# Optimization experiments

Hardware: AMD Instinct MI355X
Metric: run time of the kernel (lower is better)

## Reference

```python
import jax, jax.numpy as jnp
import numpy as np

M_IND = 1024   # inducing points
K_NN = 16      # nearest neighbors
JITTER = 1e-4


def rbf(X, Z):
    # unit-variance, unit-lengthscale RBF kernel; returns (K, squared distances)
    sq = jnp.sum(X * X, -1)[:, None] + jnp.sum(Z * Z, -1)[None, :] - 2.0 * (X @ Z.T)
    sq = jnp.maximum(sq, 0.0)
    return jnp.exp(-0.5 * sq), sq


def setup_inputs() -> dict:
    key = jax.random.key(0)
    k1, k2, k3 = jax.random.split(key, 3)
    return {
        "X": jax.random.normal(k1, (65536, 3), jnp.float32),
        "Z": jax.random.normal(k2, (M_IND, 3), jnp.float32),
        "Lu_raw": jax.random.normal(k3, (M_IND, M_IND), jnp.float32),
        "mu": jnp.zeros((M_IND,), jnp.float32),
    }


def reference(X, Z, Lu_raw, mu):
    N = X.shape[0]
    Kxx = jnp.ones((N,), X.dtype)                      # diag of RBF(X,X) is 1
    Kxz, dist = rbf(X, Z)                              # [N,M], [N,M]
    Kzz, _ = rbf(Z, Z)                                 # [M,M]

    # transform_to(lower_cholesky): strict lower triangle + exp(diag)
    Lu = jnp.tril(Lu_raw, -1) + jnp.diag(jnp.exp(jnp.diag(Lu_raw)))

    eyeM = jnp.eye(M_IND, dtype=X.dtype)
    L = jnp.linalg.cholesky(Kzz + JITTER * eyeM)       # [M,M]
    Kzz_j = L @ L.T                                    # == little_L @ little_L.T math (Kzz + jitter*I)
    Su = Lu @ Lu.T                                     # full variational covariance

    # K nearest inducing points per data point (argsort(dist)[:, :K])
    _, idx = jax.lax.top_k(-dist, K_NN)                # [N,K]

    lKzz = Kzz_j[idx[:, :, None], idx[:, None, :]]     # [N,K,K] gathered submatrices
    lS = Su[idx[:, :, None], idx[:, None, :]]          # [N,K,K]
    lKxz = jnp.take_along_axis(Kxz, idx, axis=1)       # [N,K]
    lmu = mu[idx]                                      # [N,K]

    eyeK = jnp.eye(K_NN, dtype=X.dtype)
    inv = jnp.linalg.inv(lKzz + JITTER * eyeK)         # batched tiny inverses [N,K,K]
    W = jnp.einsum('nk,nkj->nj', lKxz, inv)            # [N,K]

    mean = jnp.einsum('nk,nk->n', W, lmu)              # [N]
    cov = (Kxx
           - jnp.einsum('ni,nij,nj->n', W, lKzz, W)
           + jnp.einsum('ni,nij,nj->n', W, lS, W))
    std = jnp.sqrt(jnp.clip(cov, 0.05, None))          # qF scale = clamp(cov, 0.05)**0.5
    return jnp.stack([mean, std])                      # [2,N] qF parameters
```

## Files before the change

kernel.cpp:

```cpp
#include <hip/hip_runtime.h>
#include <math.h>

#define N_PTS 65536
#define M_IND 1024
#define KNN 16
#define JITTER 1e-4f

#define PACKED_FLOATS (M_IND * (M_IND + 1) / 2)
#define PACKED_BYTES  ((size_t)PACKED_FLOATS * sizeof(float))

#define TSU 32
#define SU_BLOCKS 528
#define PTS_PER_BLK 128
#define QSTRIDE 17
#define GRID_BLKS (N_PTS / PTS_PER_BLK)

__device__ __forceinline__ void su_tile(const float* __restrict__ Lu_raw,
                                        float* __restrict__ P,
                                        int bid, int tid,
                                        float (*As)[36], float (*Bs)[36]) {
    int rt = (int)((sqrtf(8.0f * (float)bid + 1.0f) - 1.0f) * 0.5f);
    while ((rt + 1) * (rt + 2) / 2 <= bid) ++rt;
    while (rt * (rt + 1) / 2 > bid) --rt;
    int ct = bid - rt * (rt + 1) / 2;
    int i0 = rt * TSU, j0 = ct * TSU;

    int tx = tid & 15, ty = tid >> 4;
    int sr = tid >> 3, sc = (tid & 7) << 2;
    float a00 = 0.f, a01 = 0.f, a10 = 0.f, a11 = 0.f;

    int nch = ct + 1;
    int gi = i0 + sr, gj = j0 + sr;
    float4 pa = *(const float4*)(Lu_raw + (unsigned)gi * M_IND + sc);
    float4 pb = *(const float4*)(Lu_raw + (unsigned)gj * M_IND + sc);

    for (int c = 0; c < nch; ++c) {
        int gk = (c << 5) + sc;
        float aa[4] = {pa.x, pa.y, pa.z, pa.w};
        float bb[4] = {pb.x, pb.y, pb.z, pb.w};
        #pragma unroll
        for (int q = 0; q < 4; ++q) {
            int k = gk + q;
            aa[q] = (k < gi) ? aa[q] : ((k == gi) ? __expf(aa[q]) : 0.0f);
            bb[q] = (k < gj) ? bb[q] : ((k == gj) ? __expf(bb[q]) : 0.0f);
        }
        *(float4*)&As[sr][sc] = make_float4(aa[0], aa[1], aa[2], aa[3]);
        *(float4*)&Bs[sr][sc] = make_float4(bb[0], bb[1], bb[2], bb[3]);
        __syncthreads();
        if (c + 1 < nch) {
            int kn = ((c + 1) << 5) + sc;
            pa = *(const float4*)(Lu_raw + (unsigned)gi * M_IND + kn);
            pb = *(const float4*)(Lu_raw + (unsigned)gj * M_IND + kn);
        }
        #pragma unroll
        for (int kk = 0; kk < 32; kk += 4) {
            float4 av0 = *(const float4*)&As[ty][kk];
            float4 av1 = *(const float4*)&As[ty + 16][kk];
            float4 bv0 = *(const float4*)&Bs[tx][kk];
            float4 bv1 = *(const float4*)&Bs[tx + 16][kk];
            a00 = fmaf(av0.x, bv0.x, fmaf(av0.y, bv0.y, fmaf(av0.z, bv0.z, fmaf(av0.w, bv0.w, a00))));
            a01 = fmaf(av0.x, bv1.x, fmaf(av0.y, bv1.y, fmaf(av0.z, bv1.z, fmaf(av0.w, bv1.w, a01))));
            a10 = fmaf(av1.x, bv0.x, fmaf(av1.y, bv0.y, fmaf(av1.z, bv0.z, fmaf(av1.w, bv0.w, a10))));
            a11 = fmaf(av1.x, bv1.x, fmaf(av1.y, bv1.y, fmaf(av1.z, bv1.z, fmaf(av1.w, bv1.w, a11))));
        }
        __syncthreads();
    }

    int ia = i0 + ty, ib = i0 + ty + 16;
    int ja = j0 + tx, jb = j0 + tx + 16;
    if (ja <= ia) P[((unsigned)ia * (ia + 1) >> 1) + ja] = a00;
    if (jb <= ia) P[((unsigned)ia * (ia + 1) >> 1) + jb] = a01;
    if (ja <= ib) P[((unsigned)ib * (ib + 1) >> 1) + ja] = a10;
    if (jb <= ib) P[((unsigned)ib * (ib + 1) >> 1) + jb] = a11;
}

__global__ __launch_bounds__(256) void su_kernel(const float* __restrict__ Lu_raw,
                                                 float* __restrict__ P) {
    __shared__ float As[TSU][36];
    __shared__ float Bs[TSU][36];
    su_tile(Lu_raw, P, blockIdx.x, threadIdx.x, As, Bs);
}

__device__ __forceinline__ void ce(unsigned long long& x, unsigned long long& y) {
    unsigned long long a = x, b = y;
    bool c = a < b;
    x = c ? a : b;
    y = c ? b : a;
}
__device__ __forceinline__ void ce(float& x, float& y) {
    float a = fminf(x, y), b = fmaxf(x, y);
    x = a; y = b;
}

template <typename KT>
__device__ __forceinline__ void sort16(KT* a) {
    #pragma unroll
    for (int p = 1; p < 16; p <<= 1)
        #pragma unroll
        for (int k = p; k >= 1; k >>= 1)
            #pragma unroll
            for (int j = k & (p - 1); j + k < 16; j += 2 * k)
                #pragma unroll
                for (int i = 0; i < k; ++i)
                    if (i + j + k < 16)
                        if (((i + j) / (2 * p)) == ((i + j + k) / (2 * p)))
                            ce(a[i + j], a[i + j + k]);
}

template <typename KT>
__device__ __forceinline__ void cleanup16(KT* a) {
    #pragma unroll
    for (int d = 8; d >= 1; d >>= 1)
        #pragma unroll
        for (int i = 0; i < 16; ++i)
            if ((i & d) == 0) ce(a[i], a[i | d]);
}

__device__ __forceinline__ float distf(float4 z, float x0, float x1, float x2, float xq) {
    float dot = fmaf(x0, z.x, fmaf(x1, z.y, x2 * z.z));
    return fmaxf(fmaf(-2.0f, dot, xq + z.w), 0.0f);
}

template <int MODE>
__global__ __launch_bounds__(256, 2) void vnngp_kernel(const float* __restrict__ X,
                                                       const float* __restrict__ Z,
                                                       const float* __restrict__ mu,
                                                       float* __restrict__ P,
                                                       const float* __restrict__ Lu_raw,
                                                       unsigned int* __restrict__ ctr,
                                                       float* __restrict__ out) {
    __shared__ __align__(16) char smem[37888];
    float4* Zs = (float4*)smem;
    float* mus = (float*)(smem + 16384);
    unsigned long long* qb = (unsigned long long*)(smem + 20480);
    int tid = threadIdx.x;

    for (int r = tid; r < M_IND; r += 256) {
        float zx = Z[r * 3 + 0], zy = Z[r * 3 + 1], zz = Z[r * 3 + 2];
        Zs[r] = make_float4(zx, zy, zz, zx * zx + zy * zy + zz * zz);
        mus[r] = mu[r];
    }

    if (MODE == 2) {
        float (*As)[36] = (float (*)[36])(smem + 20480);
        float (*Bs)[36] = (float (*)[36])(smem + 20480 + 4608);
        int t = blockIdx.x;
        #pragma unroll
        for (int r = 16; r < 32; ++r) {
            int s = (r * (r + 1)) >> 1;
            if (t >= s) ++t;
        }
        su_tile(Lu_raw, P, t, tid, As, Bs);
        if (blockIdx.x < 16) {
            int r = 16 + blockIdx.x;
            su_tile(Lu_raw, P, (r * (r + 1)) >> 1, tid, As, Bs);
        }
        __syncthreads();
        if (tid == 0) {
            __threadfence();
            atomicAdd(ctr, 1u);
        }
    } else {
        __syncthreads();
    }

    {
        int pt = tid >> 2, sub = tid & 3;
        int nA = blockIdx.x * PTS_PER_BLK + pt;
        int nB = nA + 64;
        float xA0 = X[nA * 3 + 0], xA1 = X[nA * 3 + 1], xA2 = X[nA * 3 + 2];
        float xB0 = X[nB * 3 + 0], xB1 = X[nB * 3 + 1], xB2 = X[nB * 3 + 2];
        float xqA = fmaf(xA0, xA0, fmaf(xA1, xA1, xA2 * xA2));
        float xqB = fmaf(xB0, xB0, fmaf(xB1, xB1, xB2 * xB2));
        int mbase = sub << 8;
        int rot = sub << 1;

        float TA[16], TB[16];
        #pragma unroll
        for (int j = 0; j < 16; ++j) { TA[j] = 3.4e38f; TB[j] = 3.4e38f; }
        #pragma unroll 1
        for (int c = 0; c < 16; ++c) {
            int base = mbase + (c << 4);
            #pragma unroll
            for (int j = 0; j < 16; ++j) {
                int m = base + ((j + rot) & 15);
                float4 z = Zs[m];
                TA[j] = fminf(TA[j], distf(z, xA0, xA1, xA2, xqA));
                TB[j] = fminf(TB[j], distf(z, xB0, xB1, xB2, xqB));
            }
        }
        sort16(TA);
        sort16(TB);
        #pragma unroll
        for (int round = 1; round <= 2; round <<= 1) {
            float oA[16], oB[16];
            #pragma unroll
            for (int i = 0; i < 16; ++i) {
                oA[i] = __shfl_xor(TA[i], round, 64);
                oB[i] = __shfl_xor(TB[i], round, 64);
            }
            #pragma unroll
            for (int i = 0; i < 16; ++i) {
                TA[i] = fminf(TA[i], oA[15 - i]);
                TB[i] = fminf(TB[i], oB[15 - i]);
            }
            cleanup16(TA);
            cleanup16(TB);
        }
        float TstarA = TA[15], TstarB = TB[15];

        unsigned short* mycA = ((unsigned short*)qb) + pt * (QSTRIDE * 4) + sub * 16;
        unsigned short* mycB = ((unsigned short*)qb) + (pt + 64) * (QSTRIDE * 4) + sub * 16;
        int cntA = 0, cntB = 0;
        #pragma unroll 1
        for (int c = 0; c < 16; ++c) {
            int base = mbase + (c << 4);
            #pragma unroll
            for (int j = 0; j < 16; ++j) {
                int m = base + ((j + rot) & 15);
                float4 z = Zs[m];
                float dA = distf(z, xA0, xA1, xA2, xqA);
                float dB = distf(z, xB0, xB1, xB2, xqB);
                if (dA <= TstarA) { if (cntA < 16) mycA[cntA] = (unsigned short)m; ++cntA; }
                if (dB <= TstarB) { if (cntB < 16) mycB[cntB] = (unsigned short)m; ++cntB; }
            }
        }

        int ovfA = cntA > 16 ? 1 : 0;
        ovfA |= __shfl_xor(ovfA, 1, 64);
        ovfA |= __shfl_xor(ovfA, 2, 64);
        int ovfB = cntB > 16 ? 1 : 0;
        ovfB |= __shfl_xor(ovfB, 1, 64);
        ovfB |= __shfl_xor(ovfB, 2, 64);

        if (!ovfA) {
            const unsigned long long* m64 = (const unsigned long long*)mycA;
            unsigned long long raw[4] = {m64[0], m64[1], m64[2], m64[3]};
            unsigned long long C[16];
            #pragma unroll
            for (int i = 0; i < 16; ++i) {
                int m = (int)((raw[i >> 2] >> ((i & 3) * 16)) & 0x3FF);
                float d = distf(Zs[m], xA0, xA1, xA2, xqA);
                unsigned long long key =
                    ((unsigned long long)__float_as_uint(d) << 32) | (unsigned)m;
                C[i] = (i < cntA) ? key : ~0ULL;
            }
            sort16(C);
            #pragma unroll
            for (int round = 1; round <= 2; round <<= 1) {
                unsigned long long o[16];
                #pragma unroll
                for (int i = 0; i < 16; ++i) o[i] = __shfl_xor(C[i], round, 64);
                #pragma unroll
                for (int i = 0; i < 16; ++i) {
                    unsigned long long b = o[15 - i];
                    C[i] = C[i] < b ? C[i] : b;
                }
                cleanup16(C);
            }
            if (sub == 0) {
                #pragma unroll
                for (int i = 0; i < 16; ++i) qb[pt * QSTRIDE + i] = C[i];
            }
        } else if (sub == 0) {
            unsigned long long R[16];
            #pragma unroll
            for (int i = 0; i < 16; ++i) R[i] = ~0ULL;
            for (int m = 0; m < M_IND; ++m) {
                float d = distf(Zs[m], xA0, xA1, xA2, xqA);
                unsigned long long kk =
                    ((unsigned long long)__float_as_uint(d) << 32) | (unsigned)m;
                if (kk < R[15]) {
                    #pragma unroll
                    for (int j = 0; j < 16; ++j) {
                        unsigned long long t = R[j];
                        bool cc = kk < t;
                        R[j] = cc ? kk : t;
                        kk = cc ? t : kk;
                    }
                }
            }
            #pragma unroll
            for (int i = 0; i < 16; ++i) qb[pt * QSTRIDE + i] = R[i];
        }

        if (!ovfB) {
            const unsigned long long* m64 = (const unsigned long long*)mycB;
            unsigned long long raw[4] = {m64[0], m64[1], m64[2], m64[3]};
            unsigned long long C[16];
            #pragma unroll
            for (int i = 0; i < 16; ++i) {
                int m = (int)((raw[i >> 2] >> ((i & 3) * 16)) & 0x3FF);
                float d = distf(Zs[m], xB0, xB1, xB2, xqB);
                unsigned long long key =
                    ((unsigned long long)__float_as_uint(d) << 32) | (unsigned)m;
                C[i] = (i < cntB) ? key : ~0ULL;
            }
            sort16(C);
            #pragma unroll
            for (int round = 1; round <= 2; round <<= 1) {
                unsigned long long o[16];
                #pragma unroll
                for (int i = 0; i < 16; ++i) o[i] = __shfl_xor(C[i], round, 64);
                #pragma unroll
                for (int i = 0; i < 16; ++i) {
                    unsigned long long b = o[15 - i];
                    C[i] = C[i] < b ? C[i] : b;
                }
                cleanup16(C);
            }
            if (sub == 0) {
                #pragma unroll
                for (int i = 0; i < 16; ++i) qb[(pt + 64) * QSTRIDE + i] = C[i];
            }
        } else if (sub == 0) {
            unsigned long long R[16];
            #pragma unroll
            for (int i = 0; i < 16; ++i) R[i] = ~0ULL;
            for (int m = 0; m < M_IND; ++m) {
                float d = distf(Zs[m], xB0, xB1, xB2, xqB);
                unsigned long long kk =
                    ((unsigned long long)__float_as_uint(d) << 32) | (unsigned)m;
                if (kk < R[15]) {
                    #pragma unroll
                    for (int j = 0; j < 16; ++j) {
                        unsigned long long t = R[j];
                        bool cc = kk < t;
                        R[j] = cc ? kk : t;
                        kk = cc ? t : kk;
                    }
                }
            }
            #pragma unroll
            for (int i = 0; i < 16; ++i) qb[(pt + 64) * QSTRIDE + i] = R[i];
        }
    }
    __syncthreads();

    if (MODE == 2) {
        if (tid == 0) {
            while (__hip_atomic_load(ctr, __ATOMIC_ACQUIRE, __HIP_MEMORY_SCOPE_AGENT)
                   < (unsigned)GRID_BLKS)
                __builtin_amdgcn_s_sleep(8);
        }
        __syncthreads();
    }
    if (tid >= PTS_PER_BLK) return;

    int n = blockIdx.x * PTS_PER_BLK + tid;
    int idx[KNN];
    float kv[KNN];
    float nx[KNN], ny[KNN], nz[KNN], nq[KNN];
    #pragma unroll
    for (int a = 0; a < KNN; ++a) {
        unsigned long long k = qb[tid * QSTRIDE + a];
        idx[a] = (int)(k & 0xFFFFFFFFULL);
        float d = __uint_as_float((unsigned)(k >> 32));
        kv[a] = __expf(-0.5f * d);
        float4 z = Zs[idx[a]];
        nx[a] = z.x; ny[a] = z.y; nz[a] = z.z; nq[a] = z.w;
    }

    float A[KNN * (KNN + 1) / 2];
    #pragma unroll
    for (int r = 0; r < KNN; ++r) {
        A[r * (r + 1) / 2 + r] = 1.0f + 2.0f * JITTER;
        #pragma unroll
        for (int c = 0; c < r; ++c) {
            float dd = nq[r] + nq[c]
                     - 2.0f * (nx[r] * nx[c] + ny[r] * ny[c] + nz[r] * nz[c]);
            dd = fmaxf(dd, 0.0f);
            A[r * (r + 1) / 2 + c] = __expf(-0.5f * dd);
        }
    }

    #pragma unroll
    for (int c = 0; c < KNN; ++c) {
        float diag = A[c * (c + 1) / 2 + c];
        #pragma unroll
        for (int k = 0; k < c; ++k) {
            float l = A[c * (c + 1) / 2 + k];
            diag = fmaf(-l, l, diag);
        }
        float s = sqrtf(fmaxf(diag, 1e-12f));
        float rinv = 1.0f / s;
        A[c * (c + 1) / 2 + c] = rinv;
        #pragma unroll
        for (int r = c + 1; r < KNN; ++r) {
            float v = A[r * (r + 1) / 2 + c];
            #pragma unroll
            for (int k = 0; k < c; ++k)
                v = fmaf(-A[r * (r + 1) / 2 + k], A[c * (c + 1) / 2 + k], v);
            A[r * (r + 1) / 2 + c] = v * rinv;
        }
    }

    float w[KNN];
    #pragma unroll
    for (int r = 0; r < KNN; ++r) {
        float v = kv[r];
        #pragma unroll
        for (int c = 0; c < r; ++c) v = fmaf(-A[r * (r + 1) / 2 + c], w[c], v);
        w[r] = v * A[r * (r + 1) / 2 + r];
    }
    #pragma unroll
    for (int r = KNN - 1; r >= 0; --r) {
        float v = w[r];
        #pragma unroll
        for (int c = r + 1; c < KNN; ++c) v = fmaf(-A[c * (c + 1) / 2 + r], w[c], v);
        w[r] = v * A[r * (r + 1) / 2 + r];
    }

    float wk = 0.f, ww = 0.f, mean = 0.f;
    #pragma unroll
    for (int a = 0; a < KNN; ++a) {
        wk = fmaf(w[a], kv[a], wk);
        ww = fmaf(w[a], w[a], ww);
        mean = fmaf(w[a], mus[idx[a]], mean);
    }

    float qs = 0.f;
    if (MODE != 0) {
        #pragma unroll
        for (int r = 0; r < KNN; ++r) {
            int a = idx[r];
            float wr = w[r];
            float rowacc = 0.f;
            #pragma unroll
            for (int c = 0; c < r; ++c) {
                int b = idx[c];
                int hi = a > b ? a : b;
                int lo = a > b ? b : a;
                rowacc = fmaf(w[c], P[((unsigned)hi * (hi + 1) >> 1) + lo], rowacc);
            }
            qs = fmaf(wr, fmaf(wr, P[((unsigned)a * (a + 1) >> 1) + a], 2.0f * rowacc), qs);
        }
    } else {
        int si[KNN]; float sw[KNN];
        #pragma unroll
        for (int a = 0; a < KNN; ++a) { si[a] = idx[a]; sw[a] = w[a]; }
        #pragma unroll
        for (int a = 1; a < KNN; ++a) {
            int iv = si[a]; float wv = sw[a];
            int b = a - 1;
            while (b >= 0 && si[b] > iv) { si[b + 1] = si[b]; sw[b + 1] = sw[b]; --b; }
            si[b + 1] = iv; sw[b + 1] = wv;
        }
        int s = 0;
        int kend = si[KNN - 1];
        for (int k = 0; k <= kend; ++k) {
            float v = 0.f;
            if (s < KNN && si[s] == k) {
                v = sw[s] * __expf(Lu_raw[(unsigned)k * M_IND + k]);
                ++s;
            }
            for (int a = s; a < KNN; ++a)
                v = fmaf(sw[a], Lu_raw[(unsigned)si[a] * M_IND + k], v);
            qs = fmaf(v, v, qs);
        }
    }

    float cov = 1.0f - (wk - JITTER * ww) + qs;
    float sd = sqrtf(fmaxf(cov, 0.05f));
    out[n] = mean;
    out[N_PTS + n] = sd;
}

extern "C" void kernel_launch(void* const* d_in, const int* in_sizes, int n_in,
                              void* d_out, int out_size, void* d_ws, size_t ws_size,
                              hipStream_t stream) {
    const float* X      = (const float*)d_in[0];
    const float* Z      = (const float*)d_in[1];
    const float* Lu_raw = (const float*)d_in[2];
    const float* mu     = (const float*)d_in[3];
    float* out = (float*)d_out;

    if (ws_size >= PACKED_BYTES + 64) {
        float* P = (float*)d_ws;
        unsigned int* ctr = (unsigned int*)((char*)d_ws + PACKED_BYTES);
        hipMemsetAsync(ctr, 0, sizeof(unsigned int), stream);
        vnngp_kernel<2><<<GRID_BLKS, 256, 0, stream>>>(X, Z, mu, P, Lu_raw, ctr, out);
    } else if (ws_size >= PACKED_BYTES) {
        float* P = (float*)d_ws;
        su_kernel<<<SU_BLOCKS, 256, 0, stream>>>(Lu_raw, P);
        vnngp_kernel<1><<<GRID_BLKS, 256, 0, stream>>>(X, Z, mu, P, Lu_raw, nullptr, out);
    } else {
        vnngp_kernel<0><<<GRID_BLKS, 256, 0, stream>>>(X, Z, mu, nullptr, Lu_raw, nullptr, out);
    }
}
```

Before: 170.6 us.

## Halve points per block, simplify distance math, and restrict Su barrier to tile blocks

Each block now handles 64 points (one per 4-thread group) instead of two per group, doubling the grid to 1024 blocks. Shared memory shrinks and launch bounds rise to 5 blocks per CU for more occupancy. The Su tile work is given to the first 528 blocks only, and the spin-wait counts only those blocks rather than the whole grid. Distance computation is rewritten as a half-norm fused dot product, which saves a few ops in the scan and in the Kzz exponent. The risks are that a grid-wide spin wait with more blocks than can be resident at once could deadlock, and that the lost ILP from two points per thread may hurt.

```diff
diff --git a/kernel.cpp b/kernel.cpp
--- a/kernel.cpp
+++ b/kernel.cpp
@@ -11,9 +11,11 @@
 
 #define TSU 32
 #define SU_BLOCKS 528
-#define PTS_PER_BLK 128
+#define PTS_PER_BLK 64
 #define QSTRIDE 17
 #define GRID_BLKS (N_PTS / PTS_PER_BLK)
+
+#define SMEM_BYTES 29696
 
 __device__ __forceinline__ void su_tile(const float* __restrict__ Lu_raw,
                                         float* __restrict__ P,
@@ -116,20 +118,19 @@
             if ((i & d) == 0) ce(a[i], a[i | d]);
 }
 
-__device__ __forceinline__ float distf(float4 z, float x0, float x1, float x2, float xq) {
-    float dot = fmaf(x0, z.x, fmaf(x1, z.y, x2 * z.z));
-    return fmaxf(fmaf(-2.0f, dot, xq + z.w), 0.0f);
+__device__ __forceinline__ float uval(float4 z, float xn0, float xn1, float xn2) {
+    return fmaf(xn0, z.x, fmaf(xn1, z.y, fmaf(xn2, z.z, z.w)));
 }
 
 template <int MODE>
-__global__ __launch_bounds__(256, 2) void vnngp_kernel(const float* __restrict__ X,
+__global__ __launch_bounds__(256, 5) void vnngp_kernel(const float* __restrict__ X,
                                                        const float* __restrict__ Z,
                                                        const float* __restrict__ mu,
                                                        float* __restrict__ P,
                                                        const float* __restrict__ Lu_raw,
                                                        unsigned int* __restrict__ ctr,
                                                        float* __restrict__ out) {
-    __shared__ __align__(16) char smem[37888];
+    __shared__ __align__(16) char smem[SMEM_BYTES];
     float4* Zs = (float4*)smem;
     float* mus = (float*)(smem + 16384);
     unsigned long long* qb = (unsigned long long*)(smem + 20480);
@@ -137,28 +138,22 @@
 
     for (int r = tid; r < M_IND; r += 256) {
         float zx = Z[r * 3 + 0], zy = Z[r * 3 + 1], zz = Z[r * 3 + 2];
-        Zs[r] = make_float4(zx, zy, zz, zx * zx + zy * zy + zz * zz);
+        Zs[r] = make_float4(zx, zy, zz, 0.5f * (zx * zx + zy * zy + zz * zz));
         mus[r] = mu[r];
     }
 
     if (MODE == 2) {
-        float (*As)[36] = (float (*)[36])(smem + 20480);
-        float (*Bs)[36] = (float (*)[36])(smem + 20480 + 4608);
-        int t = blockIdx.x;
-        #pragma unroll
-        for (int r = 16; r < 32; ++r) {
-            int s = (r * (r + 1)) >> 1;
-            if (t >= s) ++t;
-        }
-        su_tile(Lu_raw, P, t, tid, As, Bs);
-        if (blockIdx.x < 16) {
-            int r = 16 + blockIdx.x;
-            su_tile(Lu_raw, P, (r * (r + 1)) >> 1, tid, As, Bs);
-        }
-        __syncthreads();
-        if (tid == 0) {
-            __threadfence();
-            atomicAdd(ctr, 1u);
+        if (blockIdx.x < SU_BLOCKS) {
+            float (*As)[36] = (float (*)[36])(smem + 20480);
+            float (*Bs)[36] = (float (*)[36])(smem + 20480 + 4608);
+            su_tile(Lu_raw, P, blockIdx.x, tid, As, Bs);
+            __syncthreads();
+            if (tid == 0) {
+                __threadfence();
+                atomicAdd(ctr, 1u);
+            }
+        } else {
+            __syncthreads();
         }
     } else {
         __syncthreads();
@@ -166,18 +161,16 @@
 
     {
         int pt = tid >> 2, sub = tid & 3;
-        int nA = blockIdx.x * PTS_PER_BLK + pt;
-        int nB = nA + 64;
-        float xA0 = X[nA * 3 + 0], xA1 = X[nA * 3 + 1], xA2 = X[nA * 3 + 2];
-        float xB0 = X[nB * 3 + 0], xB1 = X[nB * 3 + 1], xB2 = X[nB * 3 + 2];
-        float xqA = fmaf(xA0, xA0, fmaf(xA1, xA1, xA2 * xA2));
-        float xqB = fmaf(xB0, xB0, fmaf(xB1, xB1, xB2 * xB2));
+        int n = blockIdx.x * PTS_PER_BLK + pt;
+        float x0 = X[n * 3 + 0], x1 = X[n * 3 + 1], x2 = X[n * 3 + 2];
+        float xq = fmaf(x0, x0, fmaf(x1, x1, x2 * x2));
+        float xn0 = -x0, xn1 = -x1, xn2 = -x2;
         int mbase = sub << 8;
         int rot = sub << 1;
 
-        float TA[16], TB[16];
-        #pragma unroll
-        for (int j = 0; j < 16; ++j) { TA[j] = 3.4e38f; TB[j] = 3.4e38f; }
+        float T[16];
+        #pragma unroll
+        for (int j = 0; j < 16; ++j) T[j] = 3.4e38f;
         #pragma unroll 1
         for (int c = 0; c < 16; ++c) {
             int base = mbase + (c << 4);
@@ -185,33 +178,23 @@
             for (int j = 0; j < 16; ++j) {
                 int m = base + ((j + rot) & 15);
                 float4 z = Zs[m];
-                TA[j] = fminf(TA[j], distf(z, xA0, xA1, xA2, xqA));
-                TB[j] = fminf(TB[j], distf(z, xB0, xB1, xB2, xqB));
-            }
-        }
-        sort16(TA);
-        sort16(TB);
+                T[j] = fminf(T[j], uval(z, xn0, xn1, xn2));
+            }
+        }
+        sort16(T);
         #pragma unroll
         for (int round = 1; round <= 2; round <<= 1) {
-            float oA[16], oB[16];
-            #pragma unroll
-            for (int i = 0; i < 16; ++i) {
-                oA[i] = __shfl_xor(TA[i], round, 64);
-                oB[i] = __shfl_xor(TB[i], round, 64);
-            }
-            #pragma unroll
-            for (int i = 0; i < 16; ++i) {
-                TA[i] = fminf(TA[i], oA[15 - i]);
-                TB[i] = fminf(TB[i], oB[15 - i]);
-            }
-            cleanup16(TA);
-            cleanup16(TB);
-        }
-        float TstarA = TA[15], TstarB = TB[15];
-
-        unsigned short* mycA = ((unsigned short*)qb) + pt * (QSTRIDE * 4) + sub * 16;
-        unsigned short* mycB = ((unsigned short*)qb) + (pt + 64) * (QSTRIDE * 4) + sub * 16;
-        int cntA = 0, cntB = 0;
+            float o[16];
+            #pragma unroll
+            for (int i = 0; i < 16; ++i) o[i] = __shfl_xor(T[i], round, 64);
+            #pragma unroll
+            for (int i = 0; i < 16; ++i) T[i] = fminf(T[i], o[15 - i]);
+            cleanup16(T);
+        }
+        float Tstar = T[15];
+
+        unsigned short* myc = ((unsigned short*)qb) + pt * (QSTRIDE * 4) + sub * 16;
+        int cnt = 0;
         #pragma unroll 1
         for (int c = 0; c < 16; ++c) {
             int base = mbase + (c << 4);
@@ -219,31 +202,27 @@
             for (int j = 0; j < 16; ++j) {
                 int m = base + ((j + rot) & 15);
                 float4 z = Zs[m];
-                float dA = distf(z, xA0, xA1, xA2, xqA);
-                float dB = distf(z, xB0, xB1, xB2, xqB);
-                if (dA <= TstarA) { if (cntA < 16) mycA[cntA] = (unsigned short)m; ++cntA; }
-                if (dB <= TstarB) { if (cntB < 16) mycB[cntB] = (unsigned short)m; ++cntB; }
-            }
-        }
-
-        int ovfA = cntA > 16 ? 1 : 0;
-        ovfA |= __shfl_xor(ovfA, 1, 64);
-        ovfA |= __shfl_xor(ovfA, 2, 64);
-        int ovfB = cntB > 16 ? 1 : 0;
-        ovfB |= __shfl_xor(ovfB, 1, 64);
-        ovfB |= __shfl_xor(ovfB, 2, 64);
-
-        if (!ovfA) {
-            const unsigned long long* m64 = (const unsigned long long*)mycA;
+                float u = uval(z, xn0, xn1, xn2);
+                if (u <= Tstar) { if (cnt < 16) myc[cnt] = (unsigned short)m; ++cnt; }
+            }
+        }
+
+        int ovf = cnt > 16 ? 1 : 0;
+        ovf |= __shfl_xor(ovf, 1, 64);
+        ovf |= __shfl_xor(ovf, 2, 64);
+
+        if (!ovf) {
+            const unsigned long long* m64 = (const unsigned long long*)myc;
             unsigned long long raw[4] = {m64[0], m64[1], m64[2], m64[3]};
             unsigned long long C[16];
             #pragma unroll
             for (int i = 0; i < 16; ++i) {
                 int m = (int)((raw[i >> 2] >> ((i & 3) * 16)) & 0x3FF);
-                float d = distf(Zs[m], xA0, xA1, xA2, xqA);
+                float4 z = Zs[m];
+                float d = fmaxf(fmaf(2.0f, uval(z, xn0, xn1, xn2), xq), 0.0f);
                 unsigned long long key =
                     ((unsigned long long)__float_as_uint(d) << 32) | (unsigned)m;
-                C[i] = (i < cntA) ? key : ~0ULL;
+                C[i] = (i < cnt) ? key : ~0ULL;
             }
             sort16(C);
             #pragma unroll
@@ -267,7 +246,8 @@
             #pragma unroll
             for (int i = 0; i < 16; ++i) R[i] = ~0ULL;
             for (int m = 0; m < M_IND; ++m) {
-                float d = distf(Zs[m], xA0, xA1, xA2, xqA);
+                float4 z = Zs[m];
+                float d = fmaxf(fmaf(2.0f, uval(z, xn0, xn1, xn2), xq), 0.0f);
                 unsigned long long kk =
                     ((unsigned long long)__float_as_uint(d) << 32) | (unsigned)m;
                 if (kk < R[15]) {
@@ -283,64 +263,13 @@
             #pragma unroll
             for (int i = 0; i < 16; ++i) qb[pt * QSTRIDE + i] = R[i];
         }
-
-        if (!ovfB) {
-            const unsigned long long* m64 = (const unsigned long long*)mycB;
-            unsigned long long raw[4] = {m64[0], m64[1], m64[2], m64[3]};
-            unsigned long long C[16];
-            #pragma unroll
-            for (int i = 0; i < 16; ++i) {
-                int m = (int)((raw[i >> 2] >> ((i & 3) * 16)) & 0x3FF);
-                float d = distf(Zs[m], xB0, xB1, xB2, xqB);
-                unsigned long long key =
-                    ((unsigned long long)__float_as_uint(d) << 32) | (unsigned)m;
-                C[i] = (i < cntB) ? key : ~0ULL;
-            }
-            sort16(C);
-            #pragma unroll
-            for (int round = 1; round <= 2; round <<= 1) {
-                unsigned long long o[16];
-                #pragma unroll
-                for (int i = 0; i < 16; ++i) o[i] = __shfl_xor(C[i], round, 64);
-                #pragma unroll
-                for (int i = 0; i < 16; ++i) {
-                    unsigned long long b = o[15 - i];
-                    C[i] = C[i] < b ? C[i] : b;
-                }
-                cleanup16(C);
-            }
-            if (sub == 0) {
-                #pragma unroll
-                for (int i = 0; i < 16; ++i) qb[(pt + 64) * QSTRIDE + i] = C[i];
-            }
-        } else if (sub == 0) {
-            unsigned long long R[16];
-            #pragma unroll
-            for (int i = 0; i < 16; ++i) R[i] = ~0ULL;
-            for (int m = 0; m < M_IND; ++m) {
-                float d = distf(Zs[m], xB0, xB1, xB2, xqB);
-                unsigned long long kk =
-                    ((unsigned long long)__float_as_uint(d) << 32) | (unsigned)m;
-                if (kk < R[15]) {
-                    #pragma unroll
-                    for (int j = 0; j < 16; ++j) {
-                        unsigned long long t = R[j];
-                        bool cc = kk < t;
-                        R[j] = cc ? kk : t;
-                        kk = cc ? t : kk;
-                    }
-                }
-            }
-            #pragma unroll
-            for (int i = 0; i < 16; ++i) qb[(pt + 64) * QSTRIDE + i] = R[i];
-        }
     }
     __syncthreads();
 
     if (MODE == 2) {
         if (tid == 0) {
             while (__hip_atomic_load(ctr, __ATOMIC_ACQUIRE, __HIP_MEMORY_SCOPE_AGENT)
-                   < (unsigned)GRID_BLKS)
+                   < (unsigned)SU_BLOCKS)
                 __builtin_amdgcn_s_sleep(8);
         }
         __syncthreads();
@@ -367,10 +296,8 @@
         A[r * (r + 1) / 2 + r] = 1.0f + 2.0f * JITTER;
         #pragma unroll
         for (int c = 0; c < r; ++c) {
-            float dd = nq[r] + nq[c]
-                     - 2.0f * (nx[r] * nx[c] + ny[r] * ny[c] + nz[r] * nz[c]);
-            dd = fmaxf(dd, 0.0f);
-            A[r * (r + 1) / 2 + c] = __expf(-0.5f * dd);
+            float dot = fmaf(nx[r], nx[c], fmaf(ny[r], ny[c], nz[r] * nz[c]));
+            A[r * (r + 1) / 2 + c] = __expf(fminf(dot - nq[r] - nq[c], 0.0f));
         }
     }
 
```

Measured after the change: 216.5 us. 26.9% more time.
